# Optimization experiments

Hardware: AMD Instinct MI355X
Metric: run time of the kernel (lower is better)

## Reference

```python
import jax, jax.numpy as jnp
import numpy as np

V, E, NH, NL, FF, MAXLEN = 32000, 512, 8, 4, 2048, 80
B, L = 32, 80
EPS = 1e-5


def _ln(x, w, b):
    m = jnp.mean(x, axis=-1, keepdims=True)
    v = jnp.var(x, axis=-1, keepdims=True)
    return (x - m) / jnp.sqrt(v + EPS) * w + b


def _mha(q_in, kv_in, in_w, in_b, out_w, out_b, mask):
    # in_w: [3E, E] packed q/k/v like torch MultiheadAttention
    Bq, Lq, Em = q_in.shape
    Lk = kv_in.shape[1]
    hd = Em // NH
    q = q_in @ in_w[:Em].T + in_b[:Em]
    k = kv_in @ in_w[Em:2 * Em].T + in_b[Em:2 * Em]
    v = kv_in @ in_w[2 * Em:].T + in_b[2 * Em:]
    q = q.reshape(Bq, Lq, NH, hd).transpose(0, 2, 1, 3)
    k = k.reshape(Bq, Lk, NH, hd).transpose(0, 2, 1, 3)
    v = v.reshape(Bq, Lk, NH, hd).transpose(0, 2, 1, 3)
    s = jnp.einsum('bhqd,bhkd->bhqk', q, k) * (1.0 / float(np.sqrt(hd)))
    if mask is not None:
        s = s + mask
    a = jax.nn.softmax(s, axis=-1)
    o = jnp.einsum('bhqk,bhkd->bhqd', a, v).transpose(0, 2, 1, 3).reshape(Bq, Lq, Em)
    return o @ out_w.T + out_b


def _forward(caps, W_in, b_in, pos_emb, sa_in_w, sa_in_b, sa_out_w, sa_out_b,
             ca_in_w, ca_in_b, ca_out_w, ca_out_b, ff1_w, ff1_b, ff2_w, ff2_b,
             ln1_w, ln1_b, ln2_w, ln2_b, ln3_w, ln3_b, out_w, out_b):
    Bc, Lc = caps.shape
    # one-hot encode then dense Linear(vocab -> emb): semantically an embedding gather
    oh = jax.nn.one_hot(caps, V, dtype=jnp.float32)          # [B, L, V]
    x = oh @ W_in.T + b_in + pos_emb[:Lc][None]               # [B, L, E]
    mask = jnp.where(jnp.triu(jnp.ones((Lc, Lc), bool), 1), -jnp.inf, 0.0).astype(jnp.float32)
    mem = jnp.zeros((Bc, 1, E), jnp.float32)
    for i in range(NL):  # post-norm TransformerDecoderLayer (torch default, relu FFN)
        sa = _mha(x, x, sa_in_w[i], sa_in_b[i], sa_out_w[i], sa_out_b[i], mask)
        x = _ln(x + sa, ln1_w[i], ln1_b[i])
        ca = _mha(x, mem, ca_in_w[i], ca_in_b[i], ca_out_w[i], ca_out_b[i], None)
        x = _ln(x + ca, ln2_w[i], ln2_b[i])
        ff = jax.nn.relu(x @ ff1_w[i].T + ff1_b[i]) @ ff2_w[i].T + ff2_b[i]
        x = _ln(x + ff, ln3_w[i], ln3_b[i])
    return x @ out_w.T + out_b                                # [B, L, V]


def setup_inputs() -> dict:
    key = jax.random.key(0)
    ks = jax.random.split(key, 16)
    g = lambda k, shape, s=0.02: jax.random.normal(k, shape, jnp.float32) * s
    caps = jax.random.randint(ks[0], (B, L), 1, V)  # avoid pad_idx=0
    return {
        'caps': caps,
        'W_in': g(ks[1], (E, V)),
        'b_in': jnp.zeros((E,), jnp.float32),
        'pos_emb': g(ks[2], (MAXLEN, E)),
        'sa_in_w': g(ks[3], (NL, 3 * E, E)),
        'sa_in_b': jnp.zeros((NL, 3 * E), jnp.float32),
        'sa_out_w': g(ks[4], (NL, E, E)),
        'sa_out_b': jnp.zeros((NL, E), jnp.float32),
        'ca_in_w': g(ks[5], (NL, 3 * E, E)),
        'ca_in_b': jnp.zeros((NL, 3 * E), jnp.float32),
        'ca_out_w': g(ks[6], (NL, E, E)),
        'ca_out_b': jnp.zeros((NL, E), jnp.float32),
        'ff1_w': g(ks[7], (NL, FF, E)),
        'ff1_b': jnp.zeros((NL, FF), jnp.float32),
        'ff2_w': g(ks[8], (NL, E, FF)),
        'ff2_b': jnp.zeros((NL, E), jnp.float32),
        'ln1_w': jnp.ones((NL, E), jnp.float32),
        'ln1_b': jnp.zeros((NL, E), jnp.float32),
        'ln2_w': jnp.ones((NL, E), jnp.float32),
        'ln2_b': jnp.zeros((NL, E), jnp.float32),
        'ln3_w': jnp.ones((NL, E), jnp.float32),
        'ln3_b': jnp.zeros((NL, E), jnp.float32),
        'out_w': g(ks[9], (V, E)),
        'out_b': jnp.zeros((V,), jnp.float32),
    }


def reference(caps, W_in, b_in, pos_emb, sa_in_w, sa_in_b, sa_out_w, sa_out_b,
              ca_in_w, ca_in_b, ca_out_w, ca_out_b, ff1_w, ff1_b, ff2_w, ff2_b,
              ln1_w, ln1_b, ln2_w, ln2_b, ln3_w, ln3_b, out_w, out_b):
    return _forward(caps, W_in, b_in, pos_emb, sa_in_w, sa_in_b, sa_out_w, sa_out_b,
                    ca_in_w, ca_in_b, ca_out_w, ca_out_b, ff1_w, ff1_b, ff2_w, ff2_b,
                    ln1_w, ln1_b, ln2_w, ln2_b, ln3_w, ln3_b, out_w, out_b)
```

## Files before the change

kernel.cpp:

```cpp
#include <hip/hip_runtime.h>

typedef __attribute__((ext_vector_type(8))) short short8;
typedef __attribute__((ext_vector_type(4))) float floatx4;

__device__ __forceinline__ unsigned short f2bf(float f) {
  union { float f; unsigned int u; } un; un.f = f;
  unsigned int r = un.u + 0x7FFFu + ((un.u >> 16) & 1u);
  return (unsigned short)(r >> 16);
}

__device__ __forceinline__ void async_ld16(const unsigned short* g, unsigned short* l) {
  __builtin_amdgcn_global_load_lds(
      (const __attribute__((address_space(1))) void*)g,
      (__attribute__((address_space(3))) void*)l, 16, 0, 0);
}

__global__ __launch_bounds__(512, 1)
void gemm_vocab(const unsigned short* __restrict__ A, const float* __restrict__ Bf,
                const float* __restrict__ bias, float* __restrict__ C, int M, int N) {
  __shared__ __align__(16) unsigned short sB[65536];
  __shared__ __align__(16) unsigned short sA[2][4096];
  const int tid = threadIdx.x;
  const int lane = tid & 63;
  const int wave = tid >> 6;
  const int n0 = blockIdx.x * 128;
  const int fr = lane & 15;
  const int q = lane >> 4;
  const int wm = (wave >> 2) * 32;
  const int wn = (wave & 3) * 32;

  for (int ro = 0; ro < 16; ro++) {
    int rr = ro * 8 + wave;
    const float* src = Bf + (size_t)(n0 + rr) * 512 + lane * 8;
    float4 v0 = ((const float4*)src)[0];
    float4 v1 = ((const float4*)src)[1];
    short8 w;
    w[0] = (short)f2bf(v0.x); w[1] = (short)f2bf(v0.y);
    w[2] = (short)f2bf(v0.z); w[3] = (short)f2bf(v0.w);
    w[4] = (short)f2bf(v1.x); w[5] = (short)f2bf(v1.y);
    w[6] = (short)f2bf(v1.z); w[7] = (short)f2bf(v1.w);
    *(short8*)&sB[rr * 512 + ((lane ^ (rr & 7)) << 3)] = w;
  }

  auto stage_a = [&](int s, int buf) {
    int mt = s >> 3, kt = s & 7;
    int r = tid >> 3, cb = tid & 7;
    async_ld16(A + (size_t)(mt * 64 + r) * 512 + (kt << 6) + ((cb ^ (r & 7)) << 3),
               &sA[buf][wave * 512]);
  };

  floatx4 acc[2][2];
#pragma unroll
  for (int i = 0; i < 2; i++)
#pragma unroll
    for (int j = 0; j < 2; j++) acc[i][j] = (floatx4){0.f, 0.f, 0.f, 0.f};

  stage_a(0, 0);
  const int nsteps = (M >> 6) << 3;
  for (int s = 0; s < nsteps; s++) {
    __syncthreads();
    if (s + 1 < nsteps) stage_a(s + 1, (s + 1) & 1);
    const unsigned short* pA = sA[s & 1];
    const int kt = s & 7;
#pragma unroll
    for (int kk = 0; kk < 64; kk += 32) {
      const int cba = (kk >> 3) + q;
      short8 af[2], bfr[2];
#pragma unroll
      for (int t = 0; t < 2; t++) {
        int ra = wm + t * 16 + fr;
        af[t] = *(const short8*)&pA[ra * 64 + ((cba ^ (ra & 7)) << 3)];
        int rb = wn + t * 16 + fr;
        int cbi = (kt << 3) + cba;
        bfr[t] = *(const short8*)&sB[rb * 512 + ((cbi ^ (rb & 7)) << 3)];
      }
#pragma unroll
      for (int i = 0; i < 2; i++)
#pragma unroll
        for (int j = 0; j < 2; j++)
          acc[i][j] = __builtin_amdgcn_mfma_f32_16x16x32_bf16(af[i], bfr[j], acc[i][j], 0, 0, 0);
    }
    if (kt == 7) {
      const int mt = s >> 3;
#pragma unroll
      for (int i = 0; i < 2; i++)
#pragma unroll
        for (int j = 0; j < 2; j++) {
#pragma unroll
          for (int rg = 0; rg < 4; rg++) {
            int row = mt * 64 + wm + i * 16 + q * 4 + rg;
            int col = n0 + wn + j * 16 + fr;
            C[(size_t)row * N + col] = acc[i][j][rg] + bias[col];
          }
          acc[i][j] = (floatx4){0.f, 0.f, 0.f, 0.f};
        }
    }
  }
}

template<int TM, int TN, int OUT_BF16, int RELU>
__global__ __launch_bounds__(256, (TM == 32) ? 4 : (TM == 64) ? 3 : 2)
void gemm_bt(const unsigned short* __restrict__ A, const unsigned short* __restrict__ B,
             const float* __restrict__ bias, const float* __restrict__ res,
             void* __restrict__ Cout, int M, int N, int K) {
  constexpr int AELEM = TM * 64;
  constexpr int BELEM = TN * 64;
  constexpr int AIT = AELEM / 2048;
  constexpr int BIT = BELEM / 2048;
  constexpr int LPS = AIT + BIT;
  constexpr int LBN = (AIT > BIT) ? AIT : BIT;
  constexpr int FM = (TM + 31) / 32;
  constexpr int FN = TN / 32;
  __shared__ __align__(16) unsigned short sA[3][AELEM];
  __shared__ __align__(16) unsigned short sB[3][BELEM];
  const int tid = threadIdx.x;
  const int lane = tid & 63;
  const int wave = tid >> 6;

  const int gx = gridDim.x;
  const int nwg = gx * gridDim.y;
  const int ord = blockIdx.y * gx + blockIdx.x;
  const int qq = nwg >> 3, rr = nwg & 7;
  const int xcd = ord & 7, idx = ord >> 3;
  const int lin = (xcd < rr) ? (xcd * (qq + 1) + idx)
                             : (rr * (qq + 1) + (xcd - rr) * qq + idx);
  const int m0 = (lin % gx) * TM;
  const int n0 = (lin / gx) * TN;

  int a_off[AIT], b_off[BIT], lb[LBN];
#pragma unroll
  for (int it = 0; it < LBN; it++) lb[it] = it * 2048 + wave * 512;
#pragma unroll
  for (int it = 0; it < AIT; it++) {
    int e = it * 2048 + tid * 8;
    int r = e >> 6, cb = (e >> 3) & 7;
    a_off[it] = (m0 + r) * K + ((cb ^ (r & 7)) * 8);
  }
#pragma unroll
  for (int it = 0; it < BIT; it++) {
    int e = it * 2048 + tid * 8;
    int r = e >> 6, cb = (e >> 3) & 7;
    b_off[it] = (n0 + r) * K + ((cb ^ (r & 7)) * 8);
  }

  floatx4 acc[FM][FN];
#pragma unroll
  for (int i = 0; i < FM; i++)
#pragma unroll
    for (int j = 0; j < FN; j++) acc[i][j] = (floatx4){0.f, 0.f, 0.f, 0.f};

  const int nkt = K >> 6;
  const int wm = (wave >> 1) * (TM / 2);
  const int wn = (wave & 1) * (TN / 2);
  const int fr = lane & 15;
  const int q = lane >> 4;

  auto stage = [&](int kt, int buf) {
    const int k0 = kt << 6;
#pragma unroll
    for (int it = 0; it < AIT; it++) async_ld16(A + (size_t)a_off[it] + k0, &sA[buf][lb[it]]);
#pragma unroll
    for (int it = 0; it < BIT; it++) async_ld16(B + (size_t)b_off[it] + k0, &sB[buf][lb[it]]);
  };

  stage(0, 0);
  if (nkt > 1) stage(1, 1);
  if (nkt > 2) stage(2, 2);

  int buf = 0;
  for (int kt = 0; kt < nkt; kt++) {
    const int rem = nkt - 1 - kt;
    if (rem >= 2)      asm volatile("s_waitcnt vmcnt(%0)" :: "n"(2 * LPS) : "memory");
    else if (rem == 1) asm volatile("s_waitcnt vmcnt(%0)" :: "n"(LPS) : "memory");
    else               asm volatile("s_waitcnt vmcnt(0)" ::: "memory");
    __builtin_amdgcn_s_barrier();

    const unsigned short* pA = sA[buf];
    const unsigned short* pB = sB[buf];
#pragma unroll
    for (int kk = 0; kk < 64; kk += 32) {
      short8 af[FM], bfr[FN];
      const int cba = (kk >> 3) + q;
#pragma unroll
      for (int t = 0; t < FM; t++) {
        int ra = wm + t * 16 + fr;
        af[t] = *(const short8*)&pA[ra * 64 + ((cba ^ (ra & 7)) * 8)];
      }
#pragma unroll
      for (int t = 0; t < FN; t++) {
        int rb = wn + t * 16 + fr;
        bfr[t] = *(const short8*)&pB[rb * 64 + ((cba ^ (rb & 7)) * 8)];
      }
#pragma unroll
      for (int i = 0; i < FM; i++)
#pragma unroll
        for (int j = 0; j < FN; j++)
          acc[i][j] = __builtin_amdgcn_mfma_f32_16x16x32_bf16(af[i], bfr[j], acc[i][j], 0, 0, 0);
    }

    asm volatile("s_waitcnt lgkmcnt(0)" ::: "memory");
    __builtin_amdgcn_s_barrier();
    if (kt + 3 < nkt) stage(kt + 3, buf);
    buf = (buf == 2) ? 0 : buf + 1;
  }

#pragma unroll
  for (int i = 0; i < FM; i++) {
#pragma unroll
    for (int j = 0; j < FN; j++) {
#pragma unroll
      for (int rg = 0; rg < 4; rg++) {
        int row = m0 + wm + i * 16 + q * 4 + rg;
        int col = n0 + wn + j * 16 + fr;
        float v = acc[i][j][rg];
        if (bias) v += bias[col];
        if (res)  v += res[(size_t)row * N + col];
        if (RELU) v = v > 0.f ? v : 0.f;
        if (OUT_BF16) ((unsigned short*)Cout)[(size_t)row * N + col] = f2bf(v);
        else          ((float*)Cout)[(size_t)row * N + col] = v;
      }
    }
  }
}

__global__ __launch_bounds__(512)
void embed_cavec_kernel(const int* __restrict__ caps, const float* __restrict__ W_in,
                        const float* __restrict__ b_in, const float* __restrict__ pos,
                        float* __restrict__ x, unsigned short* __restrict__ xbf,
                        const float* __restrict__ ca_out_w, const float* __restrict__ ca_in_b,
                        const float* __restrict__ ca_out_b, float* __restrict__ cav) {
  int bid = blockIdx.x;
  if (bid < 2560) {
    int l = bid % 80;
    int tok = caps[bid];
    int e = threadIdx.x;
    float v = W_in[(size_t)e * 32000 + tok] + b_in[e] + pos[l * 512 + e];
    x[(size_t)bid * 512 + e] = v;
    xbf[(size_t)bid * 512 + e] = f2bf(v);
  } else {
    int wave = threadIdx.x >> 6, lane = threadIdx.x & 63;
    int g = (bid - 2560) * 8 + wave;
    int l = g >> 9, e = g & 511;
    const float* row = ca_out_w + ((size_t)l * 512 + e) * 512;
    const float* inb = ca_in_b + l * 1536 + 1024;
    float s = 0.f;
#pragma unroll
    for (int j = 0; j < 8; j++) s += row[lane + j * 64] * inb[lane + j * 64];
#pragma unroll
    for (int off = 32; off; off >>= 1) s += __shfl_xor(s, off);
    if (lane == 0) cav[g] = s + ca_out_b[l * 512 + e];
  }
}

__global__ __launch_bounds__(256)
void ln_kernel(const float* __restrict__ in, const float* __restrict__ w,
               const float* __restrict__ b, float* __restrict__ xout,
               unsigned short* __restrict__ xbf) {
  int row = blockIdx.x * 4 + (threadIdx.x >> 6);
  int lane = threadIdx.x & 63;
  const float* p = in + (size_t)row * 512;
  float vals[8];
  float s = 0.f, s2 = 0.f;
#pragma unroll
  for (int j = 0; j < 8; j++) {
    float t = p[lane + j * 64];
    vals[j] = t; s += t; s2 += t * t;
  }
#pragma unroll
  for (int off = 32; off; off >>= 1) { s += __shfl_xor(s, off); s2 += __shfl_xor(s2, off); }
  float mean = s * (1.f / 512.f);
  float inv = rsqrtf(s2 * (1.f / 512.f) - mean * mean + 1e-5f);
#pragma unroll
  for (int j = 0; j < 8; j++) {
    int c = lane + j * 64;
    float y = (vals[j] - mean) * inv * w[c] + b[c];
    xout[(size_t)row * 512 + c] = y;
    xbf[(size_t)row * 512 + c] = f2bf(y);
  }
}

__global__ __launch_bounds__(256)
void ln2x_kernel(const float* __restrict__ in, const float* __restrict__ cav,
                 const float* __restrict__ w1, const float* __restrict__ b1,
                 const float* __restrict__ w2, const float* __restrict__ b2,
                 float* __restrict__ xout, unsigned short* __restrict__ xbf) {
  int row = blockIdx.x * 4 + (threadIdx.x >> 6);
  int lane = threadIdx.x & 63;
  const float* p = in + (size_t)row * 512;
  float vals[8];
  float s = 0.f, s2 = 0.f;
#pragma unroll
  for (int j = 0; j < 8; j++) {
    float t = p[lane + j * 64];
    vals[j] = t; s += t; s2 += t * t;
  }
#pragma unroll
  for (int off = 32; off; off >>= 1) { s += __shfl_xor(s, off); s2 += __shfl_xor(s2, off); }
  float mean = s * (1.f / 512.f);
  float inv = rsqrtf(s2 * (1.f / 512.f) - mean * mean + 1e-5f);
  float s_b = 0.f, s2_b = 0.f;
#pragma unroll
  for (int j = 0; j < 8; j++) {
    int c = lane + j * 64;
    float y = (vals[j] - mean) * inv * w1[c] + b1[c] + cav[c];
    vals[j] = y; s_b += y; s2_b += y * y;
  }
#pragma unroll
  for (int off = 32; off; off >>= 1) { s_b += __shfl_xor(s_b, off); s2_b += __shfl_xor(s2_b, off); }
  float mean2 = s_b * (1.f / 512.f);
  float inv2 = rsqrtf(s2_b * (1.f / 512.f) - mean2 * mean2 + 1e-5f);
#pragma unroll
  for (int j = 0; j < 8; j++) {
    int c = lane + j * 64;
    float y = (vals[j] - mean2) * inv2 * w2[c] + b2[c];
    xout[(size_t)row * 512 + c] = y;
    xbf[(size_t)row * 512 + c] = f2bf(y);
  }
}

__global__ __launch_bounds__(256)
void attn_kernel(const unsigned short* __restrict__ qkv, unsigned short* __restrict__ o) {
  __shared__ __align__(16) unsigned short sq[80][72];
  __shared__ __align__(16) unsigned short sk[80][72];
  __shared__ __align__(16) unsigned short svT[64][96];
  __shared__ __align__(16) unsigned short sp[80][96];
  __shared__ float ss[80][84];
  const int tid = threadIdx.x;
  const int lane = tid & 63;
  const int wave = tid >> 6;
  const int bb = blockIdx.x >> 3, hh = blockIdx.x & 7;
  const unsigned short* base = qkv + (size_t)bb * 80 * 1536 + hh * 64;

  for (int idx = tid; idx < 5120; idx += 256) {
    int r = idx >> 6, c = idx & 63;
    sq[r][c] = base[r * 1536 + c];
    sk[r][c] = base[r * 1536 + 512 + c];
    svT[c][r] = base[r * 1536 + 1024 + c];
  }
  for (int idx = tid; idx < 1024; idx += 256) svT[idx >> 4][80 + (idx & 15)] = 0;
  for (int idx = tid; idx < 1280; idx += 256) sp[idx >> 4][80 + (idx & 15)] = 0;
  __syncthreads();

  const int fr = lane & 15;
  const int q = lane >> 4;

  for (int t = wave; t < 25; t += 4) {
    int i0 = (t / 5) * 16, j0 = (t % 5) * 16;
    floatx4 acc = (floatx4){0.f, 0.f, 0.f, 0.f};
#pragma unroll
    for (int kk = 0; kk < 64; kk += 32) {
      short8 a = *(const short8*)&sq[i0 + fr][kk + q * 8];
      short8 b = *(const short8*)&sk[j0 + fr][kk + q * 8];
      acc = __builtin_amdgcn_mfma_f32_16x16x32_bf16(a, b, acc, 0, 0, 0);
    }
#pragma unroll
    for (int rg = 0; rg < 4; rg++) {
      int row = i0 + q * 4 + rg, col = j0 + fr;
      ss[row][col] = (col <= row) ? acc[rg] * 0.125f : -1e30f;
    }
  }
  __syncthreads();

  if (tid < 80) {
    float mx = -1e30f;
#pragma unroll
    for (int j = 0; j < 80; j++) mx = fmaxf(mx, ss[tid][j]);
    float sum = 0.f;
#pragma unroll
    for (int j = 0; j < 80; j++) { float e = __expf(ss[tid][j] - mx); ss[tid][j] = e; sum += e; }
    float inv = 1.f / sum;
#pragma unroll
    for (int j = 0; j < 80; j++) sp[tid][j] = f2bf(ss[tid][j] * inv);
  }
  __syncthreads();

  for (int t = wave; t < 20; t += 4) {
    int i0 = (t / 4) * 16, d0 = (t % 4) * 16;
    floatx4 acc = (floatx4){0.f, 0.f, 0.f, 0.f};
#pragma unroll
    for (int kk = 0; kk < 96; kk += 32) {
      short8 a = *(const short8*)&sp[i0 + fr][kk + q * 8];
      short8 b = *(const short8*)&svT[d0 + fr][kk + q * 8];
      acc = __builtin_amdgcn_mfma_f32_16x16x32_bf16(a, b, acc, 0, 0, 0);
    }
#pragma unroll
    for (int rg = 0; rg < 4; rg++) {
      int row = i0 + q * 4 + rg;
      o[((size_t)bb * 80 + row) * 512 + hh * 64 + d0 + fr] = f2bf(acc[rg]);
    }
  }
}

__global__ __launch_bounds__(256)
void convert_all(const float* __restrict__ s0, unsigned short* __restrict__ d0,
                 const float* __restrict__ s1, unsigned short* __restrict__ d1,
                 const float* __restrict__ s2, unsigned short* __restrict__ d2,
                 const float* __restrict__ s3, unsigned short* __restrict__ d3) {
  int i = blockIdx.x * 256 + threadIdx.x;
  const float* s; unsigned short* d; int j = i;
  if (j < 786432) { s = s0; d = d0; }
  else if ((j -= 786432) < 262144) { s = s1; d = d1; }
  else if ((j -= 262144) < 1048576) { s = s2; d = d2; }
  else { j -= 1048576; s = s3; d = d3; }
  float4 v = ((const float4*)s)[j];
  ushort4 r;
  r.x = f2bf(v.x); r.y = f2bf(v.y); r.z = f2bf(v.z); r.w = f2bf(v.w);
  ((ushort4*)d)[j] = r;
}

extern "C" void kernel_launch(void* const* d_in, const int* in_sizes, int n_in,
                              void* d_out, int out_size, void* d_ws, size_t ws_size,
                              hipStream_t stream) {
  const int*   caps     = (const int*)d_in[0];
  const float* W_in     = (const float*)d_in[1];
  const float* b_in     = (const float*)d_in[2];
  const float* pos_emb  = (const float*)d_in[3];
  const float* sa_in_w  = (const float*)d_in[4];
  const float* sa_in_b  = (const float*)d_in[5];
  const float* sa_out_w = (const float*)d_in[6];
  const float* sa_out_b = (const float*)d_in[7];
  const float* ca_in_b  = (const float*)d_in[9];
  const float* ca_out_w = (const float*)d_in[10];
  const float* ca_out_b = (const float*)d_in[11];
  const float* ff1_w    = (const float*)d_in[12];
  const float* ff1_b    = (const float*)d_in[13];
  const float* ff2_w    = (const float*)d_in[14];
  const float* ff2_b    = (const float*)d_in[15];
  const float* ln1_w    = (const float*)d_in[16];
  const float* ln1_b    = (const float*)d_in[17];
  const float* ln2_w    = (const float*)d_in[18];
  const float* ln2_b    = (const float*)d_in[19];
  const float* ln3_w    = (const float*)d_in[20];
  const float* ln3_b    = (const float*)d_in[21];
  const float* out_w    = (const float*)d_in[22];
  const float* out_b    = (const float*)d_in[23];

  char* ws = (char*)d_ws;
  size_t off = 0;
  auto alloc = [&](size_t bytes) {
    void* p = ws + off;
    off += (bytes + 255) & ~(size_t)255;
    return p;
  };
  unsigned short* w_sa_in  = (unsigned short*)alloc((size_t)4 * 1536 * 512 * 2);
  unsigned short* w_sa_out = (unsigned short*)alloc((size_t)4 * 512 * 512 * 2);
  unsigned short* w_ff1    = (unsigned short*)alloc((size_t)4 * 2048 * 512 * 2);
  unsigned short* w_ff2    = (unsigned short*)alloc((size_t)4 * 512 * 2048 * 2);
  float*          x        = (float*)alloc((size_t)2560 * 512 * 4);
  unsigned short* xbf      = (unsigned short*)alloc((size_t)2560 * 512 * 2);
  float*          t        = (float*)alloc((size_t)2560 * 512 * 4);
  unsigned short* qkv      = (unsigned short*)alloc((size_t)2560 * 1536 * 2);
  unsigned short* obf      = (unsigned short*)alloc((size_t)2560 * 512 * 2);
  unsigned short* hbf      = (unsigned short*)alloc((size_t)2560 * 2048 * 2);
  float*          cav      = (float*)alloc((size_t)2048 * 4);

  convert_all<<<12288, 256, 0, stream>>>(sa_in_w, w_sa_in, sa_out_w, w_sa_out,
                                         ff1_w, w_ff1, ff2_w, w_ff2);
  embed_cavec_kernel<<<2816, 512, 0, stream>>>(caps, W_in, b_in, pos_emb, x, xbf,
                                               ca_out_w, ca_in_b, ca_out_b, cav);

  for (int i = 0; i < 4; i++) {
    gemm_bt<128, 64, 1, 0><<<dim3(20, 24), 256, 0, stream>>>(
        xbf, w_sa_in + (size_t)i * 1536 * 512, sa_in_b + i * 1536, nullptr,
        qkv, 2560, 1536, 512);
    attn_kernel<<<256, 256, 0, stream>>>(qkv, obf);
    gemm_bt<32, 64, 0, 0><<<dim3(80, 8), 256, 0, stream>>>(
        obf, w_sa_out + (size_t)i * 512 * 512, sa_out_b + i * 512, x,
        t, 2560, 512, 512);
    ln2x_kernel<<<640, 256, 0, stream>>>(t, cav + i * 512,
        ln1_w + i * 512, ln1_b + i * 512, ln2_w + i * 512, ln2_b + i * 512, x, xbf);
    gemm_bt<128, 64, 1, 1><<<dim3(20, 32), 256, 0, stream>>>(
        xbf, w_ff1 + (size_t)i * 2048 * 512, ff1_b + i * 2048, nullptr,
        hbf, 2560, 2048, 512);
    gemm_bt<32, 64, 0, 0><<<dim3(80, 8), 256, 0, stream>>>(
        hbf, w_ff2 + (size_t)i * 512 * 2048, ff2_b + i * 512, x,
        t, 2560, 512, 2048);
    ln_kernel<<<640, 256, 0, stream>>>(t, ln3_w + i * 512, ln3_b + i * 512, x, xbf);
  }

  gemm_vocab<<<250, 512, 0, stream>>>(xbf, out_w, out_b, (float*)d_out, 2560, 32000);
}
```

Before: 1.070 ms.

## Load vocab GEMM A fragments directly to registers, removing LDS staging and barriers

The vocab-projection kernel no longer stages A tiles through double-buffered LDS with async loads and a per-step __syncthreads. Each wave now loads its A fragments straight from global memory into registers, prefetching the next k-tile while the MFMAs on the current one run. The bias values are also hoisted into registers. This removes the per-step barrier and LDS traffic for A, at the cost of redundant global reads of A across waves and more register pressure, relying on cache hits.

```diff
diff --git a/kernel.cpp b/kernel.cpp
--- a/kernel.cpp
+++ b/kernel.cpp
@@ -19,7 +19,6 @@
 void gemm_vocab(const unsigned short* __restrict__ A, const float* __restrict__ Bf,
                 const float* __restrict__ bias, float* __restrict__ C, int M, int N) {
   __shared__ __align__(16) unsigned short sB[65536];
-  __shared__ __align__(16) unsigned short sA[2][4096];
   const int tid = threadIdx.x;
   const int lane = tid & 63;
   const int wave = tid >> 6;
@@ -42,11 +41,18 @@
     *(short8*)&sB[rr * 512 + ((lane ^ (rr & 7)) << 3)] = w;
   }
 
-  auto stage_a = [&](int s, int buf) {
-    int mt = s >> 3, kt = s & 7;
-    int r = tid >> 3, cb = tid & 7;
-    async_ld16(A + (size_t)(mt * 64 + r) * 512 + (kt << 6) + ((cb ^ (r & 7)) << 3),
-               &sA[buf][wave * 512]);
+  const float bias0 = bias[n0 + wn + fr];
+  const float bias1 = bias[n0 + wn + 16 + fr];
+
+  __syncthreads();
+
+  const unsigned short* aBase = A + (size_t)(wm + fr) * 512 + q * 8;
+  auto ldA = [&](int mt, int kt, short8* dst) {
+    const unsigned short* p = aBase + (size_t)(mt * 64) * 512 + (kt << 6);
+    dst[0] = *(const short8*)(p);
+    dst[1] = *(const short8*)(p + 32);
+    dst[2] = *(const short8*)(p + 16 * 512);
+    dst[3] = *(const short8*)(p + 16 * 512 + 32);
   };
 
   floatx4 acc[2][2];
@@ -55,46 +61,46 @@
 #pragma unroll
     for (int j = 0; j < 2; j++) acc[i][j] = (floatx4){0.f, 0.f, 0.f, 0.f};
 
-  stage_a(0, 0);
-  const int nsteps = (M >> 6) << 3;
-  for (int s = 0; s < nsteps; s++) {
-    __syncthreads();
-    if (s + 1 < nsteps) stage_a(s + 1, (s + 1) & 1);
-    const unsigned short* pA = sA[s & 1];
-    const int kt = s & 7;
-#pragma unroll
-    for (int kk = 0; kk < 64; kk += 32) {
-      const int cba = (kk >> 3) + q;
-      short8 af[2], bfr[2];
-#pragma unroll
-      for (int t = 0; t < 2; t++) {
-        int ra = wm + t * 16 + fr;
-        af[t] = *(const short8*)&pA[ra * 64 + ((cba ^ (ra & 7)) << 3)];
-        int rb = wn + t * 16 + fr;
-        int cbi = (kt << 3) + cba;
-        bfr[t] = *(const short8*)&sB[rb * 512 + ((cbi ^ (rb & 7)) << 3)];
+  short8 cur[4], nxt[4];
+  ldA(0, 0, cur);
+
+  const int nmt = M >> 6;
+  for (int mt = 0; mt < nmt; mt++) {
+#pragma unroll
+    for (int kt = 0; kt < 8; kt++) {
+      if (kt < 7)            ldA(mt, kt + 1, nxt);
+      else if (mt + 1 < nmt) ldA(mt + 1, 0, nxt);
+#pragma unroll
+      for (int kk01 = 0; kk01 < 2; kk01++) {
+        const int cbi = (kt << 3) + (kk01 << 2) + q;
+        short8 b0, b1;
+        {
+          int rb = wn + fr;
+          b0 = *(const short8*)&sB[rb * 512 + ((cbi ^ (rb & 7)) << 3)];
+          rb = wn + 16 + fr;
+          b1 = *(const short8*)&sB[rb * 512 + ((cbi ^ (rb & 7)) << 3)];
+        }
+        acc[0][0] = __builtin_amdgcn_mfma_f32_16x16x32_bf16(cur[kk01], b0, acc[0][0], 0, 0, 0);
+        acc[0][1] = __builtin_amdgcn_mfma_f32_16x16x32_bf16(cur[kk01], b1, acc[0][1], 0, 0, 0);
+        acc[1][0] = __builtin_amdgcn_mfma_f32_16x16x32_bf16(cur[2 + kk01], b0, acc[1][0], 0, 0, 0);
+        acc[1][1] = __builtin_amdgcn_mfma_f32_16x16x32_bf16(cur[2 + kk01], b1, acc[1][1], 0, 0, 0);
       }
 #pragma unroll
-      for (int i = 0; i < 2; i++)
-#pragma unroll
-        for (int j = 0; j < 2; j++)
-          acc[i][j] = __builtin_amdgcn_mfma_f32_16x16x32_bf16(af[i], bfr[j], acc[i][j], 0, 0, 0);
-    }
-    if (kt == 7) {
-      const int mt = s >> 3;
-#pragma unroll
-      for (int i = 0; i < 2; i++)
-#pragma unroll
-        for (int j = 0; j < 2; j++) {
-#pragma unroll
-          for (int rg = 0; rg < 4; rg++) {
-            int row = mt * 64 + wm + i * 16 + q * 4 + rg;
-            int col = n0 + wn + j * 16 + fr;
-            C[(size_t)row * N + col] = acc[i][j][rg] + bias[col];
-          }
-          acc[i][j] = (floatx4){0.f, 0.f, 0.f, 0.f};
+      for (int u = 0; u < 4; u++) cur[u] = nxt[u];
+    }
+#pragma unroll
+    for (int i = 0; i < 2; i++)
+#pragma unroll
+      for (int j = 0; j < 2; j++) {
+        const float bj = j ? bias1 : bias0;
+#pragma unroll
+        for (int rg = 0; rg < 4; rg++) {
+          int row = mt * 64 + wm + i * 16 + q * 4 + rg;
+          int col = n0 + wn + j * 16 + fr;
+          C[(size_t)row * N + col] = acc[i][j][rg] + bj;
         }
-    }
+        acc[i][j] = (floatx4){0.f, 0.f, 0.f, 0.f};
+      }
   }
 }
 
```

Result: slower. 1.117 ms (+4.4%).
